# Optimization experiments

Measured on AMD Instinct MI355X. Metric: run time of the kernel, lower is better.

## Reference

```python
import jax, jax.numpy as jnp
import numpy as np

EPS = 1e-5  # torch BatchNorm2d default


def _signature_depth3(path):
    """Truncated (depth-3) path signature via Chen's relation.
    path: [B, P, ch] (P points). Returns [B, ch + ch^2 + ch^3] in signatory
    layout (level 1, then row-major flattened levels 2 and 3)."""
    dx = path[:, 1:] - path[:, :-1]  # [B, P-1, ch] increments
    B, _, ch = dx.shape

    def step(carry, v):
        s1, s2, s3 = carry  # [B,ch], [B,ch,ch], [B,ch,ch,ch]
        vv = v[:, :, None] * v[:, None, :]          # v (x) v
        e2 = 0.5 * vv                               # v^(x)2 / 2!
        e3 = vv[:, :, :, None] * v[:, None, None, :] / 6.0  # v^(x)3 / 3!
        n1 = s1 + v
        n2 = s2 + s1[:, :, None] * v[:, None, :] + e2
        n3 = (s3
              + s2[:, :, :, None] * v[:, None, None, :]
              + s1[:, :, None, None] * e2[:, None, :, :]
              + e3)
        return (n1, n2, n3), None

    init = (jnp.zeros((B, ch), dx.dtype),
            jnp.zeros((B, ch, ch), dx.dtype),
            jnp.zeros((B, ch, ch, ch), dx.dtype))
    (s1, s2, s3), _ = jax.lax.scan(step, init, jnp.transpose(dx, (1, 0, 2)))
    return jnp.concatenate([s1, s2.reshape(B, -1), s3.reshape(B, -1)], axis=1)


def setup_inputs() -> dict:
    key = jax.random.key(0)
    ks = jax.random.split(key, 5)
    N, C, J, T, L = 16, 64, 25, 128, 9
    sic, out_dim = 8, 64
    ch = sic + 1                      # +1 time channel
    sig_ch = ch + ch**2 + ch**3       # 819
    x = jax.random.normal(ks[0], (N, C, J, T, L), jnp.float32)
    conv_w = jax.random.normal(ks[1], (sic, C), jnp.float32) * 0.1
    conv_b = jax.random.normal(ks[2], (sic,), jnp.float32) * 0.1
    bn_gamma = jnp.ones((sic,), jnp.float32)
    bn_beta = jnp.zeros((sic,), jnp.float32)
    lin_w = jax.random.normal(ks[3], (out_dim, sig_ch), jnp.float32) * 0.03
    lin_b = jax.random.normal(ks[4], (out_dim,), jnp.float32) * 0.03
    return dict(x=x, conv_w=conv_w, conv_b=conv_b, bn_gamma=bn_gamma,
                bn_beta=bn_beta, lin_w=lin_w, lin_b=lin_b)


def reference(x, conv_w, conv_b, bn_gamma, bn_beta, lin_w, lin_b):
    N, C, J, T, L = x.shape
    # 1x1 conv over channel dim (applied to [N*L, C, J, T] in torch, which is
    # the same per-position linear map)
    y = jnp.einsum('ncjtl,oc->nojtl', x, conv_w) + conv_b[None, :, None, None, None]
    y = jax.nn.relu(y)
    # BatchNorm2d (training mode): stats over all dims except channel
    mean = y.mean(axis=(0, 2, 3, 4), keepdims=True)
    var = ((y - mean) ** 2).mean(axis=(0, 2, 3, 4), keepdims=True)
    y = ((y - mean) * jax.lax.rsqrt(var + EPS)
         * bn_gamma[None, :, None, None, None] + bn_beta[None, :, None, None, None])
    # -> [N*J*T, L, sic] stream per (n, joint, frame)
    B = N * J * T
    p = jnp.transpose(y, (0, 2, 3, 4, 1)).reshape(B, L, -1)
    # signatory.Augment(include_time=True): prepend time channel in [0, 1]
    t = jnp.broadcast_to(jnp.linspace(0.0, 1.0, L, dtype=x.dtype)[None, :, None], (B, L, 1))
    p = jnp.concatenate([t, p], axis=-1)  # [B, L, ch]
    # signature(..., basepoint=True): prepend zero point
    path = jnp.concatenate([jnp.zeros((B, 1, p.shape[-1]), p.dtype), p], axis=1)
    sig = _signature_depth3(path)          # [B, 819]
    z = sig @ lin_w.T + lin_b              # [B, out_dim]
    return jnp.transpose(z.reshape(N, J, T, -1), (0, 3, 1, 2))  # [N, C, J, T]
```

## Files before the change

kernel.cpp:

```cpp
#include <hip/hip_runtime.h>
#include <hip/hip_bf16.h>

typedef unsigned short u16;
typedef __attribute__((ext_vector_type(8))) short short8;
typedef __attribute__((ext_vector_type(4))) float f32x4;

#define N_    16
#define C_    64
#define J_    25
#define T_    128
#define L_    9
#define SIC   8
#define OUT_  64
#define BTOT  (N_*J_*T_)
#define CNT   (BTOT*L_)
#define KPAD  896
#define NKS   27
#define SPB   28

#define K1C_BLOCKS 900
#define K1BT_BLOCKS 224
#define BT_ELEMS (OUT_*KPAD)

#define PART_OFF  0
#define SS_OFF    16384
#define BT_OFF    32768
#define Y_OFF     65536
#define WS_NEED   ((size_t)(Y_OFF + BTOT*72) * 4)

__device__ __forceinline__ short to_bf16(float x) {
  union { __hip_bfloat16 h; u16 u; } cv;
  cv.h = __float2bfloat16(x);
  return (short)cv.u;
}

__global__ __launch_bounds__(256) void k1_conv(
    const float* __restrict__ x, const float* __restrict__ cw,
    const float* __restrict__ cb, const float* __restrict__ lw,
    float* __restrict__ yws, float* __restrict__ part, u16* __restrict__ Bt) {
  int tid = threadIdx.x;

  if (blockIdx.x >= K1C_BLOCKS) {
    int idx = (blockIdx.x - K1C_BLOCKS) * 256 + tid;
    if (idx < BT_ELEMS) {
      int o = idx / KPAD, k = idx % KPAD;
      float v = 0.f;
      if (k < 864) {
        int i = k / 96, p = k % 96;
        if (p < 91) {
          int orig = (p == 0) ? i : (p < 10 ? 9 + i * 9 + (p - 1) : 90 + i * 81 + (p - 10));
          v = lw[o * 819 + orig];
        }
      }
      Bt[idx] = (u16)to_bf16(v);
    }
    return;
  }

  __shared__ float wlT[C_ * SIC];
  __shared__ float bl[SIC];
  __shared__ float wsum[4][16];
  wlT[tid] = cw[(tid & 7) * C_ + (tid >> 3)];
  wlT[tid + 256] = cw[(tid & 7) * C_ + ((tid + 256) >> 3)];
  if (tid < SIC) bl[tid] = cb[tid];
  __syncthreads();

  int p0 = (blockIdx.x * 256 + tid) * 2;
  int n = p0 / 28800, rem = p0 % 28800;
  int jj = rem / 1152, tl0 = rem % 1152;
  const float* xp = x + (size_t)(n * 1600 + jj) * 1152 + tl0;

  float acc[2][8];
#pragma unroll
  for (int p = 0; p < 2; p++)
#pragma unroll
    for (int o = 0; o < 8; o++) acc[p][o] = bl[o];

#pragma unroll 8
  for (int c = 0; c < C_; c++) {
    float2 xv = *(const float2*)(xp + (size_t)c * 28800);
    float4 w0 = *(const float4*)&wlT[c * 8];
    float4 w1 = *(const float4*)&wlT[c * 8 + 4];
    acc[0][0] = fmaf(xv.x, w0.x, acc[0][0]); acc[1][0] = fmaf(xv.y, w0.x, acc[1][0]);
    acc[0][1] = fmaf(xv.x, w0.y, acc[0][1]); acc[1][1] = fmaf(xv.y, w0.y, acc[1][1]);
    acc[0][2] = fmaf(xv.x, w0.z, acc[0][2]); acc[1][2] = fmaf(xv.y, w0.z, acc[1][2]);
    acc[0][3] = fmaf(xv.x, w0.w, acc[0][3]); acc[1][3] = fmaf(xv.y, w0.w, acc[1][3]);
    acc[0][4] = fmaf(xv.x, w1.x, acc[0][4]); acc[1][4] = fmaf(xv.y, w1.x, acc[1][4]);
    acc[0][5] = fmaf(xv.x, w1.y, acc[0][5]); acc[1][5] = fmaf(xv.y, w1.y, acc[1][5]);
    acc[0][6] = fmaf(xv.x, w1.z, acc[0][6]); acc[1][6] = fmaf(xv.y, w1.z, acc[1][6]);
    acc[0][7] = fmaf(xv.x, w1.w, acc[0][7]); acc[1][7] = fmaf(xv.y, w1.w, acc[1][7]);
  }

  float vals[16];
#pragma unroll
  for (int q = 0; q < 16; q++) vals[q] = 0.f;
  float4* dst = (float4*)(yws + (size_t)p0 * 8);
#pragma unroll
  for (int p = 0; p < 2; p++) {
#pragma unroll
    for (int o = 0; o < 8; o++) acc[p][o] = fmaxf(acc[p][o], 0.f);
    dst[p * 2]     = make_float4(acc[p][0], acc[p][1], acc[p][2], acc[p][3]);
    dst[p * 2 + 1] = make_float4(acc[p][4], acc[p][5], acc[p][6], acc[p][7]);
#pragma unroll
    for (int o = 0; o < 8; o++) {
      vals[o] += acc[p][o];
      vals[8 + o] += acc[p][o] * acc[p][o];
    }
  }

  int lane = tid & 63, wid = tid >> 6;
#pragma unroll
  for (int v = 0; v < 16; v++) {
    float s = vals[v];
    for (int off = 32; off > 0; off >>= 1) s += __shfl_down(s, off, 64);
    if (lane == 0) wsum[wid][v] = s;
  }
  __syncthreads();
  if (tid < 16)
    part[blockIdx.x * 16 + tid] = wsum[0][tid] + wsum[1][tid] + wsum[2][tid] + wsum[3][tid];
}

__global__ __launch_bounds__(256) void k2_stats(
    const float* __restrict__ part, const float* __restrict__ gamma,
    const float* __restrict__ beta, float* __restrict__ ss) {
  __shared__ float red[16][16];
  int tid = threadIdx.x;
  int val = tid & 15, grp = tid >> 4;
  float s0 = 0.f, s1 = 0.f, s2 = 0.f, s3 = 0.f;
  int b = grp;
  for (; b + 48 < K1C_BLOCKS; b += 64) {
    s0 += part[b * 16 + val];
    s1 += part[(b + 16) * 16 + val];
    s2 += part[(b + 32) * 16 + val];
    s3 += part[(b + 48) * 16 + val];
  }
  for (; b < K1C_BLOCKS; b += 16) s0 += part[b * 16 + val];
  red[grp][val] = (s0 + s1) + (s2 + s3);
  __syncthreads();
  if (tid < 16) {
    float tot = 0.f;
#pragma unroll
    for (int g = 0; g < 16; g++) tot += red[g][tid];
    red[0][tid] = tot;
  }
  __syncthreads();
  if (tid < 8) {
    float mean = red[0][tid] * (1.f / CNT);
    float var  = red[0][8 + tid] * (1.f / CNT) - mean * mean;
    float sc = gamma[tid] * rsqrtf(var + 1e-5f);
    ss[tid] = sc;
    ss[8 + tid] = beta[tid] - mean * sc;
  }
}

#define SIG_STEP(vi_)                                                       \
  do {                                                                      \
    float aa = fmaf((vi_), (1.f / 6.f), 0.5f * s1);                         \
    float b2 = fmaf((vi_), 0.5f, s1);                                       \
    _Pragma("unroll")                                                       \
    for (int jj = 0; jj < 9; jj++) {                                        \
      float tj = fmaf(aa, v[jj], s2[jj]);                                   \
      _Pragma("unroll")                                                     \
      for (int kk = 0; kk < 9; kk++)                                        \
        s3[jj * 9 + kk] = fmaf(tj, v[kk], s3[jj * 9 + kk]);                 \
      s2[jj] = fmaf(b2, v[jj], s2[jj]);                                     \
    }                                                                       \
    s1 += (vi_);                                                            \
  } while (0)

__global__ __launch_bounds__(256, 3) void k3_fused(
    const float* __restrict__ yws, const float* __restrict__ ss,
    const u16* __restrict__ Bt, const float* __restrict__ lb,
    float* __restrict__ out) {
  __shared__ __align__(16) u16 sig_lds[29 * KPAD];
  __shared__ float ssl[16];
  __shared__ float lbl[64];
  float* ylds = (float*)sig_lds;
  int tid = threadIdx.x;
  if (tid < 16) ssl[tid] = ss[tid];
  if (tid >= 64 && tid < 128) lbl[tid - 64] = lb[tid - 64];
  int gBase = blockIdx.x * SPB;
  int valid = BTOT - gBase; if (valid > SPB) valid = SPB;
  __syncthreads();

  if (tid < SPB * 9) {
    int s = tid / 9;
    if (s < valid) {
      const float4* src = (const float4*)(yws + (size_t)gBase * 72 + (size_t)tid * 8);
      float4 a = src[0], b = src[1];
      float* drow = ylds + tid * 8;
      drow[0] = fmaf(a.x, ssl[0], ssl[8]);
      drow[1] = fmaf(a.y, ssl[1], ssl[9]);
      drow[2] = fmaf(a.z, ssl[2], ssl[10]);
      drow[3] = fmaf(a.w, ssl[3], ssl[11]);
      drow[4] = fmaf(b.x, ssl[4], ssl[12]);
      drow[5] = fmaf(b.y, ssl[5], ssl[13]);
      drow[6] = fmaf(b.z, ssl[6], ssl[14]);
      drow[7] = fmaf(b.w, ssl[7], ssl[15]);
    }
  }
  {
    short8 z = {0, 0, 0, 0, 0, 0, 0, 0};
    int padChunks = (29 - valid) * 112;
    for (int e = tid; e < padChunks; e += 256) {
      int r = valid + e / 112, sl = e % 112;
      *(short8*)&sig_lds[r * KPAD + sl * 8] = z;
    }
  }
  __syncthreads();

  int s = tid / 9, i = tid % 9;
  bool act = (tid < SPB * 9) && (s < valid);
  float s1 = 0.f, s2[9], s3[81];
#pragma unroll
  for (int jj = 0; jj < 9; jj++) s2[jj] = 0.f;
#pragma unroll
  for (int q = 0; q < 81; q++) s3[q] = 0.f;
  if (act) {
    const float* yrow = ylds + s * 72;
    int i1 = (i == 0) ? 0 : (i - 1);
    float prevvi;
    {
      float4 a4 = *(const float4*)(yrow);
      float4 b4 = *(const float4*)(yrow + 4);
      float v[9] = {0.f, a4.x, a4.y, a4.z, a4.w, b4.x, b4.y, b4.z, b4.w};
      float curvi = (i == 0) ? 0.f : yrow[i1];
      SIG_STEP(curvi);
      prevvi = curvi;
    }
#pragma unroll 1
    for (int l = 1; l < 9; l++) {
      float4 a4 = *(const float4*)(yrow + l * 8);
      float4 b4 = *(const float4*)(yrow + l * 8 + 4);
      float4 p4 = *(const float4*)(yrow + (l - 1) * 8);
      float4 q4 = *(const float4*)(yrow + (l - 1) * 8 + 4);
      float v[9];
      v[0] = 0.125f;
      v[1] = a4.x - p4.x; v[2] = a4.y - p4.y; v[3] = a4.z - p4.z; v[4] = a4.w - p4.w;
      v[5] = b4.x - q4.x; v[6] = b4.y - q4.y; v[7] = b4.z - q4.z; v[8] = b4.w - q4.w;
      float curvi = (i == 0) ? (float)l * 0.125f : yrow[l * 8 + i1];
      float vi = curvi - prevvi;
      prevvi = curvi;
      SIG_STEP(vi);
    }
  }
  __syncthreads();

  if (act) {
    u16* rowbase = sig_lds + s * KPAD;
    int sw = s & 7;
    {
      short8 ch;
      ch[0] = to_bf16(s1);
#pragma unroll
      for (int w = 0; w < 7; w++) ch[w + 1] = to_bf16(s2[w]);
      *(short8*)&rowbase[(((i * 12 + 0) ^ sw) * 8)] = ch;
    }
    {
      short8 ch;
      ch[0] = to_bf16(s2[7]); ch[1] = to_bf16(s2[8]);
#pragma unroll
      for (int w = 0; w < 6; w++) ch[w + 2] = to_bf16(s3[w]);
      *(short8*)&rowbase[(((i * 12 + 1) ^ sw) * 8)] = ch;
    }
#pragma unroll
    for (int c = 2; c <= 10; c++) {
      short8 ch;
#pragma unroll
      for (int w = 0; w < 8; w++) ch[w] = to_bf16(s3[c * 8 - 10 + w]);
      *(short8*)&rowbase[(((i * 12 + c) ^ sw) * 8)] = ch;
    }
    {
      short8 ch;
      ch[0] = to_bf16(s3[78]); ch[1] = to_bf16(s3[79]); ch[2] = to_bf16(s3[80]);
      ch[3] = 0; ch[4] = 0; ch[5] = 0; ch[6] = 0; ch[7] = 0;
      *(short8*)&rowbase[(((i * 12 + 11) ^ sw) * 8)] = ch;
    }
  }
  __syncthreads();

  int w = tid >> 6, l = tid & 63;
  int brow = (w << 4) + (l & 15);
  const short8* bp = (const short8*)(Bt + (size_t)brow * KPAD);
  int arow0 = (l & 15);
  int arow1 = 16 + (l & 15); if (arow1 > 28) arow1 = 28;
  int asw0 = arow0 & 7, asw1 = arow1 & 7;
  f32x4 acc0 = {0, 0, 0, 0}, acc1 = {0, 0, 0, 0};
#pragma unroll
  for (int ks = 0; ks < NKS; ks++) {
    int s4 = ks * 4 + (l >> 4);
    short8 bfrag = bp[s4];
    short8 a0 = *(const short8*)&sig_lds[arow0 * KPAD + ((s4 ^ asw0) * 8)];
    short8 a1 = *(const short8*)&sig_lds[arow1 * KPAD + ((s4 ^ asw1) * 8)];
    acc0 = __builtin_amdgcn_mfma_f32_16x16x32_bf16(a0, bfrag, acc0, 0, 0, 0);
    acc1 = __builtin_amdgcn_mfma_f32_16x16x32_bf16(a1, bfrag, acc1, 0, 0, 0);
  }
  __syncthreads();

  float* c_lds = (float*)sig_lds;
  int o = (w << 4) + (l & 15);
#pragma unroll
  for (int r = 0; r < 4; r++) {
    int m0 = (l >> 4) * 4 + r;
    c_lds[o * 33 + m0] = acc0[r];
    c_lds[o * 33 + 16 + m0] = acc1[r];
  }
  __syncthreads();
  for (int e = tid; e < 2048; e += 256) {
    int o2 = e >> 5, m = e & 31;
    if (m < valid) {
      int b = gBase + m;
      int n = b / (J_ * T_), rem = b % (J_ * T_);
      int j = rem >> 7, t = rem & (T_ - 1);
      out[(((size_t)n * OUT_ + o2) * J_ + j) * T_ + t] = c_lds[o2 * 33 + m] + lbl[o2];
    }
  }
}

extern "C" void kernel_launch(void* const* d_in, const int* in_sizes, int n_in,
                              void* d_out, int out_size, void* d_ws, size_t ws_size,
                              hipStream_t stream) {
  const float* x     = (const float*)d_in[0];
  const float* cw    = (const float*)d_in[1];
  const float* cb    = (const float*)d_in[2];
  const float* gamma = (const float*)d_in[3];
  const float* beta  = (const float*)d_in[4];
  const float* lw    = (const float*)d_in[5];
  const float* lbias = (const float*)d_in[6];
  float* out = (float*)d_out;
  float* ws  = (float*)d_ws;
  if (ws_size < WS_NEED) return;

  float* part = ws + PART_OFF;
  float* ss   = ws + SS_OFF;
  u16*   bt   = (u16*)(ws + BT_OFF);
  float* yws  = ws + Y_OFF;

  hipLaunchKernelGGL(k1_conv, dim3(K1C_BLOCKS + K1BT_BLOCKS), dim3(256), 0, stream,
                     x, cw, cb, lw, yws, part, bt);
  hipLaunchKernelGGL(k2_stats, dim3(1), dim3(256), 0, stream, part, gamma, beta, ss);

  int nblk3 = (BTOT + SPB - 1) / SPB;
  hipLaunchKernelGGL(k3_fused, dim3(nblk3), dim3(256), 0, stream, yws, ss, bt, lbias, out);
}
```

Baseline: 71.60 us.

## Fuse BN stats reduction into conv kernel via last-block atomic, prefetch MFMA operands

The separate single-block stats kernel is removed. The conv kernel now uses a global atomic counter so the last finishing block reduces the per-block partials and writes the BN scale and shift. The conv grid becomes 1024 blocks with 225 active threads each, so the partial count is a multiple of 64. In the signature kernel, the yws loads are issued before the first barrier, and the MFMA loop double-buffers its B and A fragments to hide load latency. The cost is an extra memset launch plus atomics and fences, and 31 idle lanes per conv block.

```diff
diff --git a/kernel.cpp b/kernel.cpp
--- a/kernel.cpp
+++ b/kernel.cpp
@@ -18,12 +18,14 @@
 #define NKS   27
 #define SPB   28
 
-#define K1C_BLOCKS 900
+#define K1C_BLOCKS 1024
+#define K1_ACT     225
 #define K1BT_BLOCKS 224
 #define BT_ELEMS (OUT_*KPAD)
 
 #define PART_OFF  0
-#define SS_OFF    16384
+#define CNT_OFF   16384
+#define SS_OFF    24576
 #define BT_OFF    32768
 #define Y_OFF     65536
 #define WS_NEED   ((size_t)(Y_OFF + BTOT*72) * 4)
@@ -37,7 +39,10 @@
 __global__ __launch_bounds__(256) void k1_conv(
     const float* __restrict__ x, const float* __restrict__ cw,
     const float* __restrict__ cb, const float* __restrict__ lw,
-    float* __restrict__ yws, float* __restrict__ part, u16* __restrict__ Bt) {
+    const float* __restrict__ gamma, const float* __restrict__ beta,
+    float* __restrict__ yws, float* __restrict__ part,
+    unsigned int* __restrict__ cnt, float* __restrict__ ss,
+    u16* __restrict__ Bt) {
   int tid = threadIdx.x;
 
   if (blockIdx.x >= K1C_BLOCKS) {
@@ -60,51 +65,56 @@
   __shared__ float wlT[C_ * SIC];
   __shared__ float bl[SIC];
   __shared__ float wsum[4][16];
+  __shared__ float red2[16][16];
+  __shared__ int isLast;
   wlT[tid] = cw[(tid & 7) * C_ + (tid >> 3)];
   wlT[tid + 256] = cw[(tid & 7) * C_ + ((tid + 256) >> 3)];
   if (tid < SIC) bl[tid] = cb[tid];
   __syncthreads();
 
-  int p0 = (blockIdx.x * 256 + tid) * 2;
-  int n = p0 / 28800, rem = p0 % 28800;
-  int jj = rem / 1152, tl0 = rem % 1152;
-  const float* xp = x + (size_t)(n * 1600 + jj) * 1152 + tl0;
-
-  float acc[2][8];
-#pragma unroll
-  for (int p = 0; p < 2; p++)
-#pragma unroll
-    for (int o = 0; o < 8; o++) acc[p][o] = bl[o];
+  float vals[16];
+#pragma unroll
+  for (int q = 0; q < 16; q++) vals[q] = 0.f;
+
+  if (tid < K1_ACT) {
+    int p0 = (blockIdx.x * K1_ACT + tid) * 2;
+    int n = p0 / 28800, rem = p0 % 28800;
+    int jj = rem / 1152, tl0 = rem % 1152;
+    const float* xp = x + (size_t)(n * 1600 + jj) * 1152 + tl0;
+
+    float acc[2][8];
+#pragma unroll
+    for (int p = 0; p < 2; p++)
+#pragma unroll
+      for (int o = 0; o < 8; o++) acc[p][o] = bl[o];
 
 #pragma unroll 8
-  for (int c = 0; c < C_; c++) {
-    float2 xv = *(const float2*)(xp + (size_t)c * 28800);
-    float4 w0 = *(const float4*)&wlT[c * 8];
-    float4 w1 = *(const float4*)&wlT[c * 8 + 4];
-    acc[0][0] = fmaf(xv.x, w0.x, acc[0][0]); acc[1][0] = fmaf(xv.y, w0.x, acc[1][0]);
-    acc[0][1] = fmaf(xv.x, w0.y, acc[0][1]); acc[1][1] = fmaf(xv.y, w0.y, acc[1][1]);
-    acc[0][2] = fmaf(xv.x, w0.z, acc[0][2]); acc[1][2] = fmaf(xv.y, w0.z, acc[1][2]);
-    acc[0][3] = fmaf(xv.x, w0.w, acc[0][3]); acc[1][3] = fmaf(xv.y, w0.w, acc[1][3]);
-    acc[0][4] = fmaf(xv.x, w1.x, acc[0][4]); acc[1][4] = fmaf(xv.y, w1.x, acc[1][4]);
-    acc[0][5] = fmaf(xv.x, w1.y, acc[0][5]); acc[1][5] = fmaf(xv.y, w1.y, acc[1][5]);
-    acc[0][6] = fmaf(xv.x, w1.z, acc[0][6]); acc[1][6] = fmaf(xv.y, w1.z, acc[1][6]);
-    acc[0][7] = fmaf(xv.x, w1.w, acc[0][7]); acc[1][7] = fmaf(xv.y, w1.w, acc[1][7]);
-  }
-
-  float vals[16];
-#pragma unroll
-  for (int q = 0; q < 16; q++) vals[q] = 0.f;
-  float4* dst = (float4*)(yws + (size_t)p0 * 8);
-#pragma unroll
-  for (int p = 0; p < 2; p++) {
-#pragma unroll
-    for (int o = 0; o < 8; o++) acc[p][o] = fmaxf(acc[p][o], 0.f);
-    dst[p * 2]     = make_float4(acc[p][0], acc[p][1], acc[p][2], acc[p][3]);
-    dst[p * 2 + 1] = make_float4(acc[p][4], acc[p][5], acc[p][6], acc[p][7]);
-#pragma unroll
-    for (int o = 0; o < 8; o++) {
-      vals[o] += acc[p][o];
-      vals[8 + o] += acc[p][o] * acc[p][o];
+    for (int c = 0; c < C_; c++) {
+      float2 xv = *(const float2*)(xp + (size_t)c * 28800);
+      float4 w0 = *(const float4*)&wlT[c * 8];
+      float4 w1 = *(const float4*)&wlT[c * 8 + 4];
+      acc[0][0] = fmaf(xv.x, w0.x, acc[0][0]); acc[1][0] = fmaf(xv.y, w0.x, acc[1][0]);
+      acc[0][1] = fmaf(xv.x, w0.y, acc[0][1]); acc[1][1] = fmaf(xv.y, w0.y, acc[1][1]);
+      acc[0][2] = fmaf(xv.x, w0.z, acc[0][2]); acc[1][2] = fmaf(xv.y, w0.z, acc[1][2]);
+      acc[0][3] = fmaf(xv.x, w0.w, acc[0][3]); acc[1][3] = fmaf(xv.y, w0.w, acc[1][3]);
+      acc[0][4] = fmaf(xv.x, w1.x, acc[0][4]); acc[1][4] = fmaf(xv.y, w1.x, acc[1][4]);
+      acc[0][5] = fmaf(xv.x, w1.y, acc[0][5]); acc[1][5] = fmaf(xv.y, w1.y, acc[1][5]);
+      acc[0][6] = fmaf(xv.x, w1.z, acc[0][6]); acc[1][6] = fmaf(xv.y, w1.z, acc[1][6]);
+      acc[0][7] = fmaf(xv.x, w1.w, acc[0][7]); acc[1][7] = fmaf(xv.y, w1.w, acc[1][7]);
+    }
+
+    float4* dst = (float4*)(yws + (size_t)p0 * 8);
+#pragma unroll
+    for (int p = 0; p < 2; p++) {
+#pragma unroll
+      for (int o = 0; o < 8; o++) acc[p][o] = fmaxf(acc[p][o], 0.f);
+      dst[p * 2]     = make_float4(acc[p][0], acc[p][1], acc[p][2], acc[p][3]);
+      dst[p * 2 + 1] = make_float4(acc[p][4], acc[p][5], acc[p][6], acc[p][7]);
+#pragma unroll
+      for (int o = 0; o < 8; o++) {
+        vals[o] += acc[p][o];
+        vals[8 + o] += acc[p][o] * acc[p][o];
+      }
     }
   }
 
@@ -118,35 +128,37 @@
   __syncthreads();
   if (tid < 16)
     part[blockIdx.x * 16 + tid] = wsum[0][tid] + wsum[1][tid] + wsum[2][tid] + wsum[3][tid];
-}
-
-__global__ __launch_bounds__(256) void k2_stats(
-    const float* __restrict__ part, const float* __restrict__ gamma,
-    const float* __restrict__ beta, float* __restrict__ ss) {
-  __shared__ float red[16][16];
-  int tid = threadIdx.x;
+
+  __threadfence();
+  __syncthreads();
+  if (tid == 0) {
+    unsigned int old = atomicAdd(cnt, 1u);
+    isLast = (old == K1C_BLOCKS - 1) ? 1 : 0;
+  }
+  __syncthreads();
+  if (!isLast) return;
+  __threadfence();
+
   int val = tid & 15, grp = tid >> 4;
   float s0 = 0.f, s1 = 0.f, s2 = 0.f, s3 = 0.f;
-  int b = grp;
-  for (; b + 48 < K1C_BLOCKS; b += 64) {
+  for (int b = grp; b < K1C_BLOCKS; b += 64) {
     s0 += part[b * 16 + val];
     s1 += part[(b + 16) * 16 + val];
     s2 += part[(b + 32) * 16 + val];
     s3 += part[(b + 48) * 16 + val];
   }
-  for (; b < K1C_BLOCKS; b += 16) s0 += part[b * 16 + val];
-  red[grp][val] = (s0 + s1) + (s2 + s3);
+  red2[grp][val] = (s0 + s1) + (s2 + s3);
   __syncthreads();
   if (tid < 16) {
     float tot = 0.f;
 #pragma unroll
-    for (int g = 0; g < 16; g++) tot += red[g][tid];
-    red[0][tid] = tot;
+    for (int g = 0; g < 16; g++) tot += red2[g][tid];
+    red2[0][tid] = tot;
   }
   __syncthreads();
   if (tid < 8) {
-    float mean = red[0][tid] * (1.f / CNT);
-    float var  = red[0][8 + tid] * (1.f / CNT) - mean * mean;
+    float mean = red2[0][tid] * (1.f / CNT);
+    float var  = red2[0][8 + tid] * (1.f / CNT) - mean * mean;
     float sc = gamma[tid] * rsqrtf(var + 1e-5f);
     ss[tid] = sc;
     ss[8 + tid] = beta[tid] - mean * sc;
@@ -177,28 +189,18 @@
   __shared__ float lbl[64];
   float* ylds = (float*)sig_lds;
   int tid = threadIdx.x;
+  int gBase = blockIdx.x * SPB;
+  int valid = BTOT - gBase; if (valid > SPB) valid = SPB;
+
+  int sA = tid / 9;
+  bool actA = (tid < SPB * 9) && (sA < valid);
+  float4 ya = make_float4(0.f, 0.f, 0.f, 0.f), yb = ya;
+  if (actA) {
+    const float4* src = (const float4*)(yws + (size_t)gBase * 72 + (size_t)tid * 8);
+    ya = src[0]; yb = src[1];
+  }
   if (tid < 16) ssl[tid] = ss[tid];
   if (tid >= 64 && tid < 128) lbl[tid - 64] = lb[tid - 64];
-  int gBase = blockIdx.x * SPB;
-  int valid = BTOT - gBase; if (valid > SPB) valid = SPB;
-  __syncthreads();
-
-  if (tid < SPB * 9) {
-    int s = tid / 9;
-    if (s < valid) {
-      const float4* src = (const float4*)(yws + (size_t)gBase * 72 + (size_t)tid * 8);
-      float4 a = src[0], b = src[1];
-      float* drow = ylds + tid * 8;
-      drow[0] = fmaf(a.x, ssl[0], ssl[8]);
-      drow[1] = fmaf(a.y, ssl[1], ssl[9]);
-      drow[2] = fmaf(a.z, ssl[2], ssl[10]);
-      drow[3] = fmaf(a.w, ssl[3], ssl[11]);
-      drow[4] = fmaf(b.x, ssl[4], ssl[12]);
-      drow[5] = fmaf(b.y, ssl[5], ssl[13]);
-      drow[6] = fmaf(b.z, ssl[6], ssl[14]);
-      drow[7] = fmaf(b.w, ssl[7], ssl[15]);
-    }
-  }
   {
     short8 z = {0, 0, 0, 0, 0, 0, 0, 0};
     int padChunks = (29 - valid) * 112;
@@ -209,8 +211,21 @@
   }
   __syncthreads();
 
+  if (actA) {
+    float* drow = ylds + tid * 8;
+    drow[0] = fmaf(ya.x, ssl[0], ssl[8]);
+    drow[1] = fmaf(ya.y, ssl[1], ssl[9]);
+    drow[2] = fmaf(ya.z, ssl[2], ssl[10]);
+    drow[3] = fmaf(ya.w, ssl[3], ssl[11]);
+    drow[4] = fmaf(yb.x, ssl[4], ssl[12]);
+    drow[5] = fmaf(yb.y, ssl[5], ssl[13]);
+    drow[6] = fmaf(yb.z, ssl[6], ssl[14]);
+    drow[7] = fmaf(yb.w, ssl[7], ssl[15]);
+  }
+  __syncthreads();
+
   int s = tid / 9, i = tid % 9;
-  bool act = (tid < SPB * 9) && (s < valid);
+  bool act = actA;
   float s1 = 0.f, s2[9], s3[81];
 #pragma unroll
   for (int jj = 0; jj < 9; jj++) s2[jj] = 0.f;
@@ -277,23 +292,32 @@
       *(short8*)&rowbase[(((i * 12 + 11) ^ sw) * 8)] = ch;
     }
   }
-  __syncthreads();
 
   int w = tid >> 6, l = tid & 63;
   int brow = (w << 4) + (l & 15);
   const short8* bp = (const short8*)(Bt + (size_t)brow * KPAD);
+  int s4base = (l >> 4);
   int arow0 = (l & 15);
   int arow1 = 16 + (l & 15); if (arow1 > 28) arow1 = 28;
   int asw0 = arow0 & 7, asw1 = arow1 & 7;
+  short8 bcur = bp[s4base];
+  __syncthreads();
+
+  short8 a0c = *(const short8*)&sig_lds[arow0 * KPAD + ((s4base ^ asw0) * 8)];
+  short8 a1c = *(const short8*)&sig_lds[arow1 * KPAD + ((s4base ^ asw1) * 8)];
   f32x4 acc0 = {0, 0, 0, 0}, acc1 = {0, 0, 0, 0};
 #pragma unroll
   for (int ks = 0; ks < NKS; ks++) {
-    int s4 = ks * 4 + (l >> 4);
-    short8 bfrag = bp[s4];
-    short8 a0 = *(const short8*)&sig_lds[arow0 * KPAD + ((s4 ^ asw0) * 8)];
-    short8 a1 = *(const short8*)&sig_lds[arow1 * KPAD + ((s4 ^ asw1) * 8)];
-    acc0 = __builtin_amdgcn_mfma_f32_16x16x32_bf16(a0, bfrag, acc0, 0, 0, 0);
-    acc1 = __builtin_amdgcn_mfma_f32_16x16x32_bf16(a1, bfrag, acc1, 0, 0, 0);
+    short8 bn, a0n, a1n;
+    if (ks + 1 < NKS) {
+      int s4n = (ks + 1) * 4 + s4base;
+      bn  = bp[s4n];
+      a0n = *(const short8*)&sig_lds[arow0 * KPAD + ((s4n ^ asw0) * 8)];
+      a1n = *(const short8*)&sig_lds[arow1 * KPAD + ((s4n ^ asw1) * 8)];
+    }
+    acc0 = __builtin_amdgcn_mfma_f32_16x16x32_bf16(a0c, bcur, acc0, 0, 0, 0);
+    acc1 = __builtin_amdgcn_mfma_f32_16x16x32_bf16(a1c, bcur, acc1, 0, 0, 0);
+    if (ks + 1 < NKS) { bcur = bn; a0c = a0n; a1c = a1n; }
   }
   __syncthreads();
 
@@ -332,13 +356,14 @@
   if (ws_size < WS_NEED) return;
 
   float* part = ws + PART_OFF;
+  unsigned int* cnt = (unsigned int*)(ws + CNT_OFF);
   float* ss   = ws + SS_OFF;
   u16*   bt   = (u16*)(ws + BT_OFF);
   float* yws  = ws + Y_OFF;
 
+  hipMemsetAsync(cnt, 0, sizeof(unsigned int), stream);
   hipLaunchKernelGGL(k1_conv, dim3(K1C_BLOCKS + K1BT_BLOCKS), dim3(256), 0, stream,
-                     x, cw, cb, lw, yws, part, bt);
-  hipLaunchKernelGGL(k2_stats, dim3(1), dim3(256), 0, stream, part, gamma, beta, ss);
+                     x, cw, cb, lw, gamma, beta, yws, part, cnt, ss, bt);
 
   int nblk3 = (BTOT + SPB - 1) / SPB;
   hipLaunchKernelGGL(k3_fused, dim3(nblk3), dim3(256), 0, stream, yws, ss, bt, lbias, out);
```

New measurement: 185.2 us. 159% more time.
